# Kernel tuning notes

Measured on AMD Instinct MI355X. Metric: run time of the kernel, lower is better.

## Reference

```python
import jax, jax.numpy as jnp
import numpy as np

M = 1024   # memory_length
C = 1024   # context_length
H = 16     # num_heads
HD = 64    # head_dim = features // num_heads


def _relative_shift(x):
    # x: [B, H, T, K] -> Transformer-XL relative shift trick
    b, h, q_len, k_len = x.shape
    x = jnp.pad(x, ((0, 0), (0, 0), (0, 0), (1, 0)))
    x = x.reshape(b, h, k_len + 1, q_len)[:, :, 1:, :]
    return x.reshape(b, h, q_len, k_len)


def setup_inputs() -> dict:
    key = jax.random.key(0)
    ks = jax.random.split(key, 12)
    B, T, F = 2, C, H * HD
    S = M + C
    w = 0.02  # init scale for params
    return {
        "x": jax.random.normal(ks[0], (B, T, F), jnp.float32),
        "mask": jnp.zeros((B, T), jnp.int32),
        "mem_state": jax.random.normal(ks[1], (B, M, F), jnp.float32),
        "mem_mask": jnp.zeros((B, M), jnp.int32),
        "cache_key": jax.random.normal(ks[2], (B, C, H, HD), jnp.float32),
        "cache_value": jax.random.normal(ks[3], (B, C, H, HD), jnp.float32),
        "cache_mask": jnp.zeros((B, C), jnp.int32),
        "rel_emb": jax.random.normal(ks[4], (S, F), jnp.float32),
        "Wq": jax.random.normal(ks[5], (F, H, HD), jnp.float32) * w,
        "Wk": jax.random.normal(ks[6], (F, H, HD), jnp.float32) * w,
        "Wv": jax.random.normal(ks[7], (F, H, HD), jnp.float32) * w,
        "Wr": jax.random.normal(ks[8], (F, H, HD), jnp.float32) * w,
        "u": jax.random.normal(ks[9], (H, HD), jnp.float32) * w,
        "v": jax.random.normal(ks[10], (H, HD), jnp.float32) * w,
        "Wo": jax.random.normal(ks[11], (H, HD, F), jnp.float32) * w,
    }


def reference(x, mask, mem_state, mem_mask, cache_key, cache_value, cache_mask,
              rel_emb, Wq, Wk, Wv, Wr, u, v, Wo):
    B, T, F = x.shape
    S = M + C
    scale = 1.0 / jnp.sqrt(jnp.float32(HD))

    # projections
    q = jnp.einsum('btf,fnh->btnh', x, Wq)                       # [B,T,H,hd]
    kv_in = jnp.concatenate([mem_state, x], axis=1)              # [B,M+T,F]
    k = jnp.einsum('bsf,fnh->bsnh', kv_in, Wk)
    k = jnp.concatenate([k[:, :-T], cache_key, k[:, -T:]], axis=1)[:, -S:]   # [B,S,H,hd]
    val = jnp.einsum('bsf,fnh->bsnh', kv_in, Wv)
    val = jnp.concatenate([val[:, :-T], cache_value, val[:, -T:]], axis=1)[:, -S:]
    r = jnp.einsum('mf,fnh->mnh', rel_emb, Wr)                   # [S,H,hd]

    # relative position bias (shift trick), already scaled by 1/sqrt(hd)
    bd = jnp.einsum('btnh,mnh->bntm', q + v[None, None], r)      # [B,H,T,S]
    bd = _relative_shift(bd)[..., -S:]
    bias = bd * scale

    # segment mask from cumsum of start flags
    q_seg = jnp.cumsum(mask.astype(jnp.int32), axis=1) + \
        jnp.max(jnp.cumsum(jnp.concatenate([mem_mask, cache_mask], axis=1), axis=1), axis=1)[:, None]
    k_seg = jnp.cumsum(jnp.concatenate([mem_mask, cache_mask, mask], axis=1).astype(jnp.int32), axis=1)[:, -S:]
    seg_mask = q_seg[:, None, :, None] == k_seg[:, None, None, :]   # [B,1,T,S]

    # causal mask over absolute positions
    q_pos = jnp.arange(T) + S
    k_pos = jnp.arange(S + T)[-S:]
    causal = q_pos[:, None] >= k_pos[None, :]                    # [T,S]
    full_mask = seg_mask & causal[None, None]                    # [B,1,T,S] broadcast to H

    logits = jnp.einsum('btnh,bsnh->bnts', q + u[None, None], k) * scale + bias
    logits = jnp.where(full_mask, logits, jnp.float32(-1e30))
    attn = jax.nn.softmax(logits, axis=-1)                       # [B,H,T,S]

    o = jnp.einsum('bnts,bsnh->btnh', attn, val)
    out = jnp.einsum('btnh,nhf->btf', o, Wo)                     # [B,T,F]

    new_key = k[:, -C:]
    new_value = val[:, -C:]
    return out, new_key, new_value
```

## Files before the change

### kernel.cpp

```cpp
#include <hip/hip_runtime.h>
#include <hip/hip_bf16.h>
#include <climits>


typedef unsigned short u16;
typedef short bf16x8 __attribute__((ext_vector_type(8)));
typedef float f32x4 __attribute__((ext_vector_type(4)));

__device__ __forceinline__ f32x4 mfma16x16x32(bf16x8 a, bf16x8 b, f32x4 c) {
  return __builtin_amdgcn_mfma_f32_16x16x32_bf16(a, b, c, 0, 0, 0);
}

__device__ __forceinline__ u16 f2bf(float f) {
  __hip_bfloat16 h = __float2bfloat16(f);
  return *reinterpret_cast<u16*>(&h);
}

__device__ __forceinline__ float bf2f(u16 x) {
  unsigned u = ((unsigned)x) << 16;
  return __builtin_bit_cast(float, u);
}

__device__ __forceinline__ void gll16(const void* g, void* l) {
  __builtin_amdgcn_global_load_lds(
      (const __attribute__((address_space(1))) void*)g,
      (__attribute__((address_space(3))) void*)l, 16, 0, 0);
}

template <int CTRL>
__device__ __forceinline__ float rot16(float x) {
  int i = __builtin_bit_cast(int, x);
  int r = __builtin_amdgcn_update_dpp(i, i, CTRL, 0xF, 0xF, false);
  return __builtin_bit_cast(float, r);
}
__device__ __forceinline__ float dpp_max16(float x) {
  x = fmaxf(x, rot16<0x128>(x));
  x = fmaxf(x, rot16<0x124>(x));
  x = fmaxf(x, rot16<0x122>(x));
  x = fmaxf(x, rot16<0x121>(x));
  return x;
}
__device__ __forceinline__ float dpp_sum16(float x) {
  x += rot16<0x128>(x);
  x += rot16<0x124>(x);
  x += rot16<0x122>(x);
  x += rot16<0x121>(x);
  return x;
}

__global__ __launch_bounds__(64) void seg_scan_kernel(
    const int* __restrict__ mask, const int* __restrict__ mem_mask,
    const int* __restrict__ cache_mask, int* __restrict__ qseg,
    int* __restrict__ kseg) {
  __shared__ int cs[3072];
  int b = blockIdx.x, lane = threadIdx.x;
  int carry = 0;
  for (int base = 0; base < 3072; base += 64) {
    int idx = base + lane;
    int val;
    if (idx < 1024)      val = mem_mask[b * 1024 + idx];
    else if (idx < 2048) val = cache_mask[b * 1024 + idx - 1024];
    else                 val = mask[b * 1024 + idx - 2048];
    for (int o = 1; o < 64; o <<= 1) {
      int n = __shfl_up(val, o);
      if (lane >= o) val += n;
    }
    val += carry;
    cs[idx] = val;
    carry = __shfl(val, 63);
  }
  __syncthreads();
  int mx = INT_MIN;
  for (int i = lane; i < 2048; i += 64) mx = max(mx, cs[i]);
  for (int o = 1; o < 64; o <<= 1) mx = max(mx, __shfl_xor(mx, o));
  int cs2047 = cs[2047];
  for (int t = lane; t < 1024; t += 64) qseg[b * 1024 + t] = cs[2048 + t] - cs2047 + mx;
  for (int j = lane; j < 2048; j += 64) kseg[b * 2048 + j] = cs[1024 + j];
}

__global__ __launch_bounds__(256) void cvt2_kernel(const float* __restrict__ s0,
                                                   u16* __restrict__ d0,
                                                   const float* __restrict__ s1,
                                                   u16* __restrict__ d1) {
  int q = blockIdx.x * 256 + threadIdx.x;
  const float* s;
  u16* d;
  int i;
  if (q < 524288) { s = s0; d = d0; i = q * 4; }
  else            { s = s1; d = d1; i = (q - 524288) * 4; }
  float4 v = *(const float4*)(s + i);
  d[i + 0] = f2bf(v.x); d[i + 1] = f2bf(v.y);
  d[i + 2] = f2bf(v.z); d[i + 3] = f2bf(v.w);
}

__global__ __launch_bounds__(256) void tr_w5_kernel(
    const float* __restrict__ Wq, const float* __restrict__ Wk,
    const float* __restrict__ Wv, const float* __restrict__ Wr,
    const float* __restrict__ Wo, u16* __restrict__ wt5) {
  __shared__ float tile[32][33];
  int z = blockIdx.z;
  const float* src = (z == 0) ? Wq : (z == 1) ? Wk : (z == 2) ? Wv
                     : (z == 3) ? Wr : Wo;
  u16* dst = wt5 + ((size_t)z << 20);
  int tx = threadIdx.x & 31, ty = threadIdx.x >> 5;
  int r0 = blockIdx.y * 32, c0 = blockIdx.x * 32;
#pragma unroll
  for (int i = 0; i < 32; i += 8)
    tile[ty + i][tx] = src[(size_t)(r0 + ty + i) * 1024 + c0 + tx];
  __syncthreads();
#pragma unroll
  for (int i = 0; i < 32; i += 8)
    dst[(size_t)(c0 + ty + i) * 1024 + r0 + tx] = f2bf(tile[tx][ty + i]);
}

__global__ __launch_bounds__(256) void ck_perm_kernel(const float* __restrict__ src,
                                                      u16* __restrict__ dst) {
  int i = blockIdx.x * 256 + threadIdx.x;
  int dq = i & 15, h = (i >> 4) & 15, t = (i >> 8) & 1023, b = i >> 18;
  float4 v = *(const float4*)(src + (size_t)i * 4);
  size_t o = (((size_t)(b * 16 + h)) * 2048 + t) * 64 + dq * 4;
  dst[o + 0] = f2bf(v.x); dst[o + 1] = f2bf(v.y);
  dst[o + 2] = f2bf(v.z); dst[o + 3] = f2bf(v.w);
}

__global__ __launch_bounds__(256) void cv_tr_kernel(const float* __restrict__ src,
                                                    u16* __restrict__ dst) {
  __shared__ float tile[32][33];
  int bh = blockIdx.z, b = bh >> 4, h = bh & 15;
  int t0 = blockIdx.x * 32, d0 = blockIdx.y * 32;
  int tx = threadIdx.x & 31, ty = threadIdx.x >> 5;
#pragma unroll
  for (int i = 0; i < 32; i += 8)
    tile[ty + i][tx] = src[(((size_t)b * 1024 + t0 + ty + i) * 16 + h) * 64 + d0 + tx];
  __syncthreads();
#pragma unroll
  for (int i = 0; i < 32; i += 8)
    dst[((size_t)bh * 64 + d0 + ty + i) * 2048 + t0 + tx] = f2bf(tile[tx][ty + i]);
}

__global__ __launch_bounds__(256, 2) void gemm_proj_kernel(
    const u16* __restrict__ xbf, const u16* __restrict__ relbf,
    const u16* __restrict__ obf, const u16* __restrict__ wt5,
    u16* __restrict__ qu, u16* __restrict__ qv, u16* __restrict__ kbuf,
    u16* __restrict__ vtbuf, u16* __restrict__ rbuf, float* __restrict__ dout,
    const float* __restrict__ uvec, const float* __restrict__ vvec, int movr) {
  __shared__ __align__(16) u16 lA[128 * 64];
  __shared__ __align__(16) u16 lB[128 * 64];
  const int mode = (movr >= 0) ? movr : (int)blockIdx.z;
  const u16* A = (mode == 3) ? relbf : ((mode == 4) ? obf : xbf);
  const u16* Wm = wt5 + (size_t)mode * 1048576;
  const int tid = threadIdx.x;
  const int lane = tid & 63, gq = lane >> 4, cl = lane & 15;
  const int wv = tid >> 6, wm = wv >> 1, wn = wv & 1;
  const int by = blockIdx.y * 128, bx = blockIdx.x * 128;
  const f32x4 fz = {0.f, 0.f, 0.f, 0.f};

  f32x4 acc[4][4];
#pragma unroll
  for (int mi = 0; mi < 4; ++mi)
#pragma unroll
    for (int ni = 0; ni < 4; ++ni) acc[mi][ni] = fz;

  int offs[4];
  const u16 *pA[4], *pB[4];
#pragma unroll
  for (int c = 0; c < 4; ++c) {
    int off = tid * 16 + c * 4096;
    int L = off ^ (((off >> 7) & 7) << 4);
    int rr = off >> 7, ke = (L & 127) >> 1;
    offs[c] = off;
    pA[c] = A + (size_t)(by + rr) * 1024 + ke;
    pB[c] = Wm + (size_t)(bx + rr) * 1024 + ke;
  }

  for (int k0 = 0; k0 < 1024; k0 += 64) {
#pragma unroll
    for (int c = 0; c < 4; ++c) {
      gll16(pA[c] + k0, (char*)lA + offs[c]);
      gll16(pB[c] + k0, (char*)lB + offs[c]);
    }
    __syncthreads();
    bf16x8 af[4][2], bff[4][2];
#pragma unroll
    for (int mi = 0; mi < 4; ++mi)
#pragma unroll
      for (int kb = 0; kb < 2; ++kb) {
        int row = wm * 64 + mi * 16 + cl;
        int byte = row * 128 + kb * 64 + gq * 16;
        byte ^= ((row & 7) << 4);
        af[mi][kb] = *(const bf16x8*)((const char*)lA + byte);
      }
#pragma unroll
    for (int ni = 0; ni < 4; ++ni)
#pragma unroll
      for (int kb = 0; kb < 2; ++kb) {
        int row = wn * 64 + ni * 16 + cl;
        int byte = row * 128 + kb * 64 + gq * 16;
        byte ^= ((row & 7) << 4);
        bff[ni][kb] = *(const bf16x8*)((const char*)lB + byte);
      }
#pragma unroll
    for (int mi = 0; mi < 4; ++mi)
#pragma unroll
      for (int ni = 0; ni < 4; ++ni) {
        acc[mi][ni] = mfma16x16x32(af[mi][0], bff[ni][0], acc[mi][ni]);
        acc[mi][ni] = mfma16x16x32(af[mi][1], bff[ni][1], acc[mi][ni]);
      }
    __syncthreads();
  }

  const float SC = 0.18033688011112042f;
#pragma unroll
  for (int mi = 0; mi < 4; ++mi)
#pragma unroll
    for (int ni = 0; ni < 4; ++ni) {
      int n = bx + wn * 64 + ni * 16 + cl;
      float ub = 0.f, vb = 0.f;
      if (mode == 0) { ub = uvec[n]; vb = vvec[n]; }
#pragma unroll
      for (int r = 0; r < 4; ++r) {
        int m = by + wm * 64 + mi * 16 + 4 * gq + r;
        float val = acc[mi][ni][r];
        if (mode == 0) {
          qu[(size_t)m * 1024 + n] = f2bf((val + ub) * SC);
          qv[(size_t)m * 1024 + n] = f2bf((val + vb) * SC);
        } else if (mode == 1) {
          dout[2097152 + (size_t)m * 1024 + n] = val;
          kbuf[(((size_t)((m >> 10) * 16 + (n >> 6))) * 2048 + 1024 + (m & 1023)) * 64 +
               (n & 63)] = f2bf(val);
        } else if (mode == 2) {
          dout[4194304 + (size_t)m * 1024 + n] = val;
          vtbuf[(((size_t)((m >> 10) * 16 + (n >> 6))) * 64 + (n & 63)) * 2048 + 1024 +
                (m & 1023)] = f2bf(val);
        } else if (mode == 3) {
          rbuf[((size_t)(n >> 6) * 2048 + m) * 64 + (n & 63)] = f2bf(val);
        } else {
          dout[(size_t)m * 1024 + n] = val;
        }
      }
    }
}

__global__ __launch_bounds__(256, 2) void attn_kernel(
    const u16* __restrict__ qu, const u16* __restrict__ qv,
    const u16* __restrict__ kbuf, const u16* __restrict__ vtbuf,
    const u16* __restrict__ rbuf, const int* __restrict__ qseg,
    const int* __restrict__ kseg, u16* __restrict__ pO,
    float* __restrict__ pml) {
  __shared__ __align__(16) u16 ldsK[2][64 * 64];
  __shared__ __align__(16) u16 ldsV[2][64 * 64];
  __shared__ __align__(16) u16 ldsP[4][16 * 64];

  const int tid = threadIdx.x, lane = tid & 63;
  const int gq = lane >> 4, cl = lane & 15;
  const int wv = tid >> 6;
  int lin = blockIdx.x + 64 * blockIdx.y;
  lin = (lin & 7) * 256 + (lin >> 3);
  const int bh = lin >> 6, xx = lin & 63;
  const int qt = xx >> 2, chunk = xx & 3;
  const int b = bh >> 4, h = bh & 15;
  const int i0b = qt * 64;
  const int i0 = i0b + wv * 16;
  const int tmax = (i0b + 63 + 1024) >> 6;
  const f32x4 fz = {0.f, 0.f, 0.f, 0.f};

  const u16* rbh = rbuf + (size_t)h * 2048 * 64;
  const int* ksegb = kseg + (size_t)b * 2048;

  const u16* Kbase = kbuf + (size_t)bh * 2048 * 64;
  const u16* Vbase = vtbuf + (size_t)bh * 64 * 2048;
  const int offc0 = tid * 16, offc1 = tid * 16 + 4096;
  const int L0s = offc0 ^ (((offc0 >> 7) & 7) << 4);
  const int L1s = offc1 ^ (((offc1 >> 7) & 7) << 4);
  const u16* kS0 = Kbase + (size_t)(offc0 >> 7) * 64 + ((L0s & 127) >> 1);
  const u16* kS1 = Kbase + (size_t)(offc1 >> 7) * 64 + ((L1s & 127) >> 1);
  const u16* vS0 = Vbase + (size_t)(offc0 >> 7) * 2048 + ((L0s & 127) >> 1);
  const u16* vS1 = Vbase + (size_t)(offc1 >> 7) * 2048 + ((L1s & 127) >> 1);

#define STAGE(T, B)                                                \
  do {                                                             \
    gll16(kS0 + (size_t)(T) * 4096, (char*)ldsK[B] + offc0);       \
    gll16(kS1 + (size_t)(T) * 4096, (char*)ldsK[B] + offc1);       \
    gll16(vS0 + (T) * 64, (char*)ldsV[B] + offc0);                 \
    gll16(vS1 + (T) * 64, (char*)ldsV[B] + offc1);                 \
  } while (0)

  STAGE(chunk, 0);

  bf16x8 aU[2], aV[2];
#pragma unroll
  for (int kb = 0; kb < 2; ++kb) {
    size_t off = ((size_t)b * 1024 + i0 + cl) * 1024 + h * 64 + kb * 32 + gq * 8;
    aU[kb] = *(const bf16x8*)(qu + off);
    aV[kb] = *(const bf16x8*)(qv + off);
  }
  int qsv[4], srcl[4], athr[4];
  bool sel[4];
#pragma unroll
  for (int r = 0; r < 4; ++r) {
    int ri = 4 * gq + r;
    qsv[r] = qseg[b * 1024 + i0 + ri];
    int lc = cl - ri + 15;
    srcl[r] = (gq << 4) | (lc & 15);
    sel[r] = (lc < 16);
    athr[r] = i0 + ri + 1024 - cl;
  }

  float mrun[4], lrun[4];
  f32x4 oacc[4];
#pragma unroll
  for (int r = 0; r < 4; ++r) { mrun[r] = -1e30f; lrun[r] = 0.f; }
#pragma unroll
  for (int di = 0; di < 4; ++di) oacc[di] = fz;

  __syncthreads();

  int bufi = 0;
  for (int t = chunk; t <= tmax; t += 4, bufi ^= 1) {
    if (t + 4 <= tmax) STAGE(t + 4, bufi ^ 1);
    const int j0t = t * 64;
    const int Rb0 = j0t - i0 + 1008;
    bf16x8 Rf[5][2];
#pragma unroll
    for (int p = 0; p < 5; ++p) {
      const u16* rp = rbh + (size_t)min(Rb0 + 16 * p + cl, 2047) * 64 + gq * 8;
      Rf[p][0] = *(const bf16x8*)rp;
      Rf[p][1] = *(const bf16x8*)(rp + 32);
    }
    int ksv[4];
#pragma unroll
    for (int jt = 0; jt < 4; ++jt) ksv[jt] = ksegb[j0t + 16 * jt + cl];
    __builtin_amdgcn_sched_barrier(0);

    const char* Kl = (const char*)ldsK[bufi];
    const char* Vl = (const char*)ldsV[bufi];
    f32x4 xq[4];
#pragma unroll
    for (int jt = 0; jt < 4; ++jt) {
      int row = jt * 16 + cl;
      int sw = (row & 7) << 4;
      bf16x8 k0 = *(const bf16x8*)(Kl + ((row * 128 + gq * 16) ^ sw));
      bf16x8 k1 = *(const bf16x8*)(Kl + ((row * 128 + 64 + gq * 16) ^ sw));
      f32x4 a = mfma16x16x32(aU[0], k0, fz);
      xq[jt] = mfma16x16x32(aU[1], k1, a);
    }
    f32x4 bb[5];
#pragma unroll
    for (int p = 0; p < 5; ++p) {
      f32x4 a = mfma16x16x32(aV[0], Rf[p][0], fz);
      bb[p] = mfma16x16x32(aV[1], Rf[p][1], a);
    }
    float D[5][4];
#pragma unroll
    for (int p = 0; p < 5; ++p)
#pragma unroll
      for (int r = 0; r < 4; ++r) D[p][r] = __shfl(bb[p][r], srcl[r]);
    __builtin_amdgcn_sched_barrier(0);

    float x[4][4];
#pragma unroll
    for (int jt = 0; jt < 4; ++jt)
#pragma unroll
      for (int r = 0; r < 4; ++r) {
        float bdv = sel[r] ? D[jt][r] : D[jt + 1][r];
        bool ok = (j0t + 16 * jt <= athr[r]) && (ksv[jt] == qsv[r]);
        x[jt][r] = ok ? (xq[jt][r] + bdv) : -1e30f;
      }

    char* Pm = (char*)ldsP[wv];
    float alf[4];
#pragma unroll
    for (int r = 0; r < 4; ++r) {
      float mx = fmaxf(fmaxf(x[0][r], x[1][r]), fmaxf(x[2][r], x[3][r]));
      mx = dpp_max16(mx);
      float mold = mrun[r];
      float mnew = fmaxf(mold, mx);
      float al = exp2f(mold - mnew);
      float p0 = exp2f(x[0][r] - mnew);
      float p1 = exp2f(x[1][r] - mnew);
      float p2 = exp2f(x[2][r] - mnew);
      float p3 = exp2f(x[3][r] - mnew);
      float s = dpp_sum16(p0 + p1 + p2 + p3);
      mrun[r] = mnew;
      lrun[r] = lrun[r] * al + s;
      alf[r] = al;
      int ri = 4 * gq + r;
      int bbx = (ri & 7) << 4;
      *(u16*)(Pm + ((ri * 128 + cl * 2) ^ bbx)) = f2bf(p0);
      *(u16*)(Pm + ((ri * 128 + (16 + cl) * 2) ^ bbx)) = f2bf(p1);
      *(u16*)(Pm + ((ri * 128 + (32 + cl) * 2) ^ bbx)) = f2bf(p2);
      *(u16*)(Pm + ((ri * 128 + (48 + cl) * 2) ^ bbx)) = f2bf(p3);
    }
    f32x4 av = {alf[0], alf[1], alf[2], alf[3]};
#pragma unroll
    for (int di = 0; di < 4; ++di) oacc[di] *= av;
    int psw = (cl & 7) << 4;
    bf16x8 pf0 = *(const bf16x8*)(Pm + ((cl * 128 + gq * 16) ^ psw));
    bf16x8 pf1 = *(const bf16x8*)(Pm + ((cl * 128 + 64 + gq * 16) ^ psw));
#pragma unroll
    for (int di = 0; di < 4; ++di) {
      int row = di * 16 + cl;
      int sw = (row & 7) << 4;
      bf16x8 v0 = *(const bf16x8*)(Vl + ((row * 128 + gq * 16) ^ sw));
      bf16x8 v1 = *(const bf16x8*)(Vl + ((row * 128 + 64 + gq * 16) ^ sw));
      oacc[di] = mfma16x16x32(pf0, v0, oacc[di]);
      oacc[di] = mfma16x16x32(pf1, v1, oacc[di]);
    }
    __syncthreads();
  }
#undef STAGE

#pragma unroll
  for (int r = 0; r < 4; ++r) {
    int iq = i0 + 4 * gq + r;
    size_t rowp = ((size_t)bh * 4 + chunk) * 1024 + iq;
#pragma unroll
    for (int di = 0; di < 4; ++di)
      __builtin_nontemporal_store(f2bf(oacc[di][r]), &pO[rowp * 64 + di * 16 + cl]);
    if (cl == 0) {
      __builtin_nontemporal_store(mrun[r], &pml[rowp * 2]);
      __builtin_nontemporal_store(lrun[r], &pml[rowp * 2 + 1]);
    }
  }
}

__global__ __launch_bounds__(256) void combine_kernel(
    const u16* __restrict__ pO, const float* __restrict__ pml,
    u16* __restrict__ obf) {
  int gid = blockIdx.x * 256 + threadIdx.x;
  int d8 = (gid & 7) * 8;
  int row = gid >> 3;
  int bh = row >> 10, iq = row & 1023;
  int b = bh >> 4, h = bh & 15;
  size_t rbase = (size_t)bh * 4 * 1024 + iq;
  float m[4], l[4], w[4];
  float ms = -1e30f;
#pragma unroll
  for (int c = 0; c < 4; ++c) {
    m[c] = pml[(rbase + c * 1024) * 2];
    l[c] = pml[(rbase + c * 1024) * 2 + 1];
    ms = fmaxf(ms, m[c]);
  }
  float den = 0.f;
#pragma unroll
  for (int c = 0; c < 4; ++c) { w[c] = exp2f(m[c] - ms); den += l[c] * w[c]; }
  float inv = 1.0f / fmaxf(den, 1e-30f);
  float acc[8] = {0, 0, 0, 0, 0, 0, 0, 0};
#pragma unroll
  for (int c = 0; c < 4; ++c) {
    bf16x8 a = *(const bf16x8*)(pO + (rbase + c * 1024) * 64 + d8);
#pragma unroll
    for (int j = 0; j < 8; ++j) acc[j] += bf2f((u16)a[j]) * w[c];
  }
  bf16x8 o;
#pragma unroll
  for (int j = 0; j < 8; ++j) o[j] = (short)f2bf(acc[j] * inv);
  *(bf16x8*)(obf + ((size_t)b * 1024 + iq) * 1024 + h * 64 + d8) = o;
}

extern "C" void kernel_launch(void* const* d_in, const int* in_sizes, int n_in,
                              void* d_out, int out_size, void* d_ws, size_t ws_size,
                              hipStream_t stream) {
  (void)in_sizes; (void)n_in; (void)out_size; (void)ws_size;
  const float* x           = (const float*)d_in[0];
  const int*   mask        = (const int*)d_in[1];
  const int*   mem_mask    = (const int*)d_in[3];
  const float* cache_key   = (const float*)d_in[4];
  const float* cache_value = (const float*)d_in[5];
  const int*   cache_mask  = (const int*)d_in[6];
  const float* rel_emb     = (const float*)d_in[7];
  const float* Wq          = (const float*)d_in[8];
  const float* Wk          = (const float*)d_in[9];
  const float* Wv          = (const float*)d_in[10];
  const float* Wr          = (const float*)d_in[11];
  const float* uvec        = (const float*)d_in[12];
  const float* vvec        = (const float*)d_in[13];
  const float* Wo          = (const float*)d_in[14];
  float* dout = (float*)d_out;

  char* W = (char*)d_ws;
  u16* xbf   = (u16*)(W + (0u << 20));
  u16* relbf = (u16*)(W + (4u << 20));
  u16* pO    = (u16*)(W + (0u << 20));
  u16* wt5   = (u16*)(W + (8u << 20));
  u16* kbuf  = (u16*)(W + (18u << 20));
  u16* vtbuf = (u16*)(W + (26u << 20));
  u16* rbuf  = (u16*)(W + (34u << 20));
  u16* qu    = (u16*)(W + (38u << 20));
  u16* qv    = (u16*)(W + (42u << 20));
  u16* obf   = (u16*)(W + (46u << 20));
  int* qseg  = (int*)(W + (50u << 20));
  int* kseg  = (int*)(W + (50u << 20) + 8192);
  float* pml = (float*)(W + (50u << 20) + 32768);

  seg_scan_kernel<<<dim3(2), dim3(64), 0, stream>>>(mask, mem_mask, cache_mask, qseg, kseg);
  cvt2_kernel<<<dim3(4096), dim3(256), 0, stream>>>(x, xbf, rel_emb, relbf);
  tr_w5_kernel<<<dim3(32, 32, 5), dim3(256), 0, stream>>>(Wq, Wk, Wv, Wr, Wo, wt5);
  ck_perm_kernel<<<dim3(2048), dim3(256), 0, stream>>>(cache_key, kbuf);
  cv_tr_kernel<<<dim3(32, 2, 32), dim3(256), 0, stream>>>(cache_value, vtbuf);
  gemm_proj_kernel<<<dim3(8, 16, 4), dim3(256), 0, stream>>>(
      xbf, relbf, obf, wt5, qu, qv, kbuf, vtbuf, rbuf, dout, uvec, vvec, -1);
  attn_kernel<<<dim3(64, 32), dim3(256), 0, stream>>>(qu, qv, kbuf, vtbuf, rbuf,
                                                      qseg, kseg, pO, pml);
  combine_kernel<<<dim3(1024), dim3(256), 0, stream>>>(pO, pml, obf);
  gemm_proj_kernel<<<dim3(8, 16, 1), dim3(256), 0, stream>>>(
      xbf, relbf, obf, wt5, qu, qv, kbuf, vtbuf, rbuf, dout, uvec, vvec, 4);
}
```

Measured before the change: 197.1 us.

## Widen attention blocks to 128 queries, add dedicated 64x64 output-projection GEMM

The attention kernel now uses 512 threads (8 waves) per block, so each block covers 128 query rows and every staged K/V tile is shared by twice as many waves. It also skips the causal comparison on tiles that lie fully inside the causal region, and raises wave priority around the MFMA sections. The output projection moves to its own 64x64-tile GEMM kernel with a 512-block grid, so the small M=2048 GEMM occupies more CUs than the 128-tile generic kernel did. In exchange, the larger attention block needs more LDS and registers per block, which may lower occupancy, and the new GEMM has no double buffering.

```diff
diff --git a/kernel.cpp b/kernel.cpp
--- a/kernel.cpp
+++ b/kernel.cpp
@@ -140,14 +140,14 @@
 
 __global__ __launch_bounds__(256, 2) void gemm_proj_kernel(
     const u16* __restrict__ xbf, const u16* __restrict__ relbf,
-    const u16* __restrict__ obf, const u16* __restrict__ wt5,
-    u16* __restrict__ qu, u16* __restrict__ qv, u16* __restrict__ kbuf,
-    u16* __restrict__ vtbuf, u16* __restrict__ rbuf, float* __restrict__ dout,
-    const float* __restrict__ uvec, const float* __restrict__ vvec, int movr) {
+    const u16* __restrict__ wt5, u16* __restrict__ qu, u16* __restrict__ qv,
+    u16* __restrict__ kbuf, u16* __restrict__ vtbuf, u16* __restrict__ rbuf,
+    float* __restrict__ dout, const float* __restrict__ uvec,
+    const float* __restrict__ vvec) {
   __shared__ __align__(16) u16 lA[128 * 64];
   __shared__ __align__(16) u16 lB[128 * 64];
-  const int mode = (movr >= 0) ? movr : (int)blockIdx.z;
-  const u16* A = (mode == 3) ? relbf : ((mode == 4) ? obf : xbf);
+  const int mode = (int)blockIdx.z;
+  const u16* A = (mode == 3) ? relbf : xbf;
   const u16* Wm = wt5 + (size_t)mode * 1048576;
   const int tid = threadIdx.x;
   const int lane = tid & 63, gq = lane >> 4, cl = lane & 15;
@@ -232,16 +232,89 @@
           dout[4194304 + (size_t)m * 1024 + n] = val;
           vtbuf[(((size_t)((m >> 10) * 16 + (n >> 6))) * 64 + (n & 63)) * 2048 + 1024 +
                 (m & 1023)] = f2bf(val);
-        } else if (mode == 3) {
+        } else {
           rbuf[((size_t)(n >> 6) * 2048 + m) * 64 + (n & 63)] = f2bf(val);
-        } else {
-          dout[(size_t)m * 1024 + n] = val;
         }
       }
     }
 }
 
-__global__ __launch_bounds__(256, 2) void attn_kernel(
+__global__ __launch_bounds__(256, 2) void gemm_o_kernel(
+    const u16* __restrict__ obf, const u16* __restrict__ wo,
+    float* __restrict__ dout) {
+  __shared__ __align__(16) u16 lA[64 * 64];
+  __shared__ __align__(16) u16 lB[64 * 64];
+  const int tid = threadIdx.x;
+  const int lane = tid & 63, gq = lane >> 4, cl = lane & 15;
+  const int wv = tid >> 6, wm = wv >> 1, wn = wv & 1;
+  const int by = blockIdx.y * 64, bx = blockIdx.x * 64;
+  const f32x4 fz = {0.f, 0.f, 0.f, 0.f};
+
+  f32x4 acc[2][2];
+#pragma unroll
+  for (int a = 0; a < 2; ++a)
+#pragma unroll
+    for (int bq = 0; bq < 2; ++bq) acc[a][bq] = fz;
+
+  const int off0 = tid * 16, off1 = tid * 16 + 4096;
+  const int L0 = off0 ^ (((off0 >> 7) & 7) << 4);
+  const int L1 = off1 ^ (((off1 >> 7) & 7) << 4);
+  const int rr0 = off0 >> 7, ke0 = (L0 & 127) >> 1;
+  const int rr1 = off1 >> 7, ke1 = (L1 & 127) >> 1;
+  const u16* pA0 = obf + (size_t)(by + rr0) * 1024 + ke0;
+  const u16* pA1 = obf + (size_t)(by + rr1) * 1024 + ke1;
+  const u16* pB0 = wo + (size_t)(bx + rr0) * 1024 + ke0;
+  const u16* pB1 = wo + (size_t)(bx + rr1) * 1024 + ke1;
+
+  for (int k0 = 0; k0 < 1024; k0 += 64) {
+    gll16(pA0 + k0, (char*)lA + off0);
+    gll16(pA1 + k0, (char*)lA + off1);
+    gll16(pB0 + k0, (char*)lB + off0);
+    gll16(pB1 + k0, (char*)lB + off1);
+    __syncthreads();
+    bf16x8 af[2][2], bff[2][2];
+#pragma unroll
+    for (int mi = 0; mi < 2; ++mi)
+#pragma unroll
+      for (int kb = 0; kb < 2; ++kb) {
+        int row = wm * 32 + mi * 16 + cl;
+        int byte = row * 128 + kb * 64 + gq * 16;
+        byte ^= ((row & 7) << 4);
+        af[mi][kb] = *(const bf16x8*)((const char*)lA + byte);
+      }
+#pragma unroll
+    for (int ni = 0; ni < 2; ++ni)
+#pragma unroll
+      for (int kb = 0; kb < 2; ++kb) {
+        int row = wn * 32 + ni * 16 + cl;
+        int byte = row * 128 + kb * 64 + gq * 16;
+        byte ^= ((row & 7) << 4);
+        bff[ni][kb] = *(const bf16x8*)((const char*)lB + byte);
+      }
+#pragma unroll
+    for (int mi = 0; mi < 2; ++mi)
+#pragma unroll
+      for (int ni = 0; ni < 2; ++ni) {
+        acc[mi][ni] = mfma16x16x32(af[mi][0], bff[ni][0], acc[mi][ni]);
+        acc[mi][ni] = mfma16x16x32(af[mi][1], bff[ni][1], acc[mi][ni]);
+      }
+    __syncthreads();
+  }
+
+#pragma unroll
+  for (int mi = 0; mi < 2; ++mi)
+#pragma unroll
+    for (int ni = 0; ni < 2; ++ni) {
+      int n = bx + wn * 32 + ni * 16 + cl;
+#pragma unroll
+      for (int r = 0; r < 4; ++r) {
+        int m = by + wm * 32 + mi * 16 + 4 * gq + r;
+        dout[(size_t)m * 1024 + n] = acc[mi][ni][r];
+      }
+    }
+}
+
+__global__ __launch_bounds__(512, 2) void attn_kernel(
     const u16* __restrict__ qu, const u16* __restrict__ qv,
     const u16* __restrict__ kbuf, const u16* __restrict__ vtbuf,
     const u16* __restrict__ rbuf, const int* __restrict__ qseg,
@@ -249,19 +322,19 @@
     float* __restrict__ pml) {
   __shared__ __align__(16) u16 ldsK[2][64 * 64];
   __shared__ __align__(16) u16 ldsV[2][64 * 64];
-  __shared__ __align__(16) u16 ldsP[4][16 * 64];
+  __shared__ __align__(16) u16 ldsP[8][16 * 64];
 
   const int tid = threadIdx.x, lane = tid & 63;
   const int gq = lane >> 4, cl = lane & 15;
   const int wv = tid >> 6;
-  int lin = blockIdx.x + 64 * blockIdx.y;
-  lin = (lin & 7) * 256 + (lin >> 3);
-  const int bh = lin >> 6, xx = lin & 63;
-  const int qt = xx >> 2, chunk = xx & 3;
+  int lin = blockIdx.x + 32 * blockIdx.y;
+  lin = (lin & 7) * 128 + (lin >> 3);
+  const int bh = lin >> 5, xx = lin & 31;
+  const int qb = xx >> 2, chunk = xx & 3;
   const int b = bh >> 4, h = bh & 15;
-  const int i0b = qt * 64;
+  const int i0b = qb * 128;
   const int i0 = i0b + wv * 16;
-  const int tmax = (i0b + 63 + 1024) >> 6;
+  const int tmax = (i0b + 127 + 1024) >> 6;
   const f32x4 fz = {0.f, 0.f, 0.f, 0.f};
 
   const u16* rbh = rbuf + (size_t)h * 2048 * 64;
@@ -269,20 +342,15 @@
 
   const u16* Kbase = kbuf + (size_t)bh * 2048 * 64;
   const u16* Vbase = vtbuf + (size_t)bh * 64 * 2048;
-  const int offc0 = tid * 16, offc1 = tid * 16 + 4096;
-  const int L0s = offc0 ^ (((offc0 >> 7) & 7) << 4);
-  const int L1s = offc1 ^ (((offc1 >> 7) & 7) << 4);
-  const u16* kS0 = Kbase + (size_t)(offc0 >> 7) * 64 + ((L0s & 127) >> 1);
-  const u16* kS1 = Kbase + (size_t)(offc1 >> 7) * 64 + ((L1s & 127) >> 1);
-  const u16* vS0 = Vbase + (size_t)(offc0 >> 7) * 2048 + ((L0s & 127) >> 1);
-  const u16* vS1 = Vbase + (size_t)(offc1 >> 7) * 2048 + ((L1s & 127) >> 1);
-
-#define STAGE(T, B)                                                \
-  do {                                                             \
-    gll16(kS0 + (size_t)(T) * 4096, (char*)ldsK[B] + offc0);       \
-    gll16(kS1 + (size_t)(T) * 4096, (char*)ldsK[B] + offc1);       \
-    gll16(vS0 + (T) * 64, (char*)ldsV[B] + offc0);                 \
-    gll16(vS1 + (T) * 64, (char*)ldsV[B] + offc1);                 \
+  const int offc = tid * 16;
+  const int Ls = offc ^ (((offc >> 7) & 7) << 4);
+  const u16* kS = Kbase + (size_t)(offc >> 7) * 64 + ((Ls & 127) >> 1);
+  const u16* vS = Vbase + (size_t)(offc >> 7) * 2048 + ((Ls & 127) >> 1);
+
+#define STAGE(T, B)                                          \
+  do {                                                       \
+    gll16(kS + (size_t)(T) * 4096, (char*)ldsK[B] + offc);   \
+    gll16(vS + (T) * 64, (char*)ldsV[B] + offc);             \
   } while (0)
 
   STAGE(chunk, 0);
@@ -320,6 +388,7 @@
     if (t + 4 <= tmax) STAGE(t + 4, bufi ^ 1);
     const int j0t = t * 64;
     const int Rb0 = j0t - i0 + 1008;
+    const bool interior = (j0t + 63 <= i0 + 1024);
     bf16x8 Rf[5][2];
 #pragma unroll
     for (int p = 0; p < 5; ++p) {
@@ -334,6 +403,7 @@
 
     const char* Kl = (const char*)ldsK[bufi];
     const char* Vl = (const char*)ldsV[bufi];
+    __builtin_amdgcn_s_setprio(1);
     f32x4 xq[4];
 #pragma unroll
     for (int jt = 0; jt < 4; ++jt) {
@@ -350,6 +420,7 @@
       f32x4 a = mfma16x16x32(aV[0], Rf[p][0], fz);
       bb[p] = mfma16x16x32(aV[1], Rf[p][1], a);
     }
+    __builtin_amdgcn_s_setprio(0);
     float D[5][4];
 #pragma unroll
     for (int p = 0; p < 5; ++p)
@@ -363,7 +434,7 @@
 #pragma unroll
       for (int r = 0; r < 4; ++r) {
         float bdv = sel[r] ? D[jt][r] : D[jt + 1][r];
-        bool ok = (j0t + 16 * jt <= athr[r]) && (ksv[jt] == qsv[r]);
+        bool ok = (interior || (j0t + 16 * jt <= athr[r])) && (ksv[jt] == qsv[r]);
         x[jt][r] = ok ? (xq[jt][r] + bdv) : -1e30f;
       }
 
@@ -397,6 +468,7 @@
     int psw = (cl & 7) << 4;
     bf16x8 pf0 = *(const bf16x8*)(Pm + ((cl * 128 + gq * 16) ^ psw));
     bf16x8 pf1 = *(const bf16x8*)(Pm + ((cl * 128 + 64 + gq * 16) ^ psw));
+    __builtin_amdgcn_s_setprio(1);
 #pragma unroll
     for (int di = 0; di < 4; ++di) {
       int row = di * 16 + cl;
@@ -406,6 +478,7 @@
       oacc[di] = mfma16x16x32(pf0, v0, oacc[di]);
       oacc[di] = mfma16x16x32(pf1, v1, oacc[di]);
     }
+    __builtin_amdgcn_s_setprio(0);
     __syncthreads();
   }
 #undef STAGE
@@ -499,10 +572,9 @@
   ck_perm_kernel<<<dim3(2048), dim3(256), 0, stream>>>(cache_key, kbuf);
   cv_tr_kernel<<<dim3(32, 2, 32), dim3(256), 0, stream>>>(cache_value, vtbuf);
   gemm_proj_kernel<<<dim3(8, 16, 4), dim3(256), 0, stream>>>(
-      xbf, relbf, obf, wt5, qu, qv, kbuf, vtbuf, rbuf, dout, uvec, vvec, -1);
-  attn_kernel<<<dim3(64, 32), dim3(256), 0, stream>>>(qu, qv, kbuf, vtbuf, rbuf,
+      xbf, relbf, wt5, qu, qv, kbuf, vtbuf, rbuf, dout, uvec, vvec);
+  attn_kernel<<<dim3(32, 32), dim3(512), 0, stream>>>(qu, qv, kbuf, vtbuf, rbuf,
                                                       qseg, kseg, pO, pml);
   combine_kernel<<<dim3(1024), dim3(256), 0, stream>>>(pO, pml, obf);
-  gemm_proj_kernel<<<dim3(8, 16, 1), dim3(256), 0, stream>>>(
-      xbf, relbf, obf, wt5, qu, qv, kbuf, vtbuf, rbuf, dout, uvec, vvec, 4);
-}
+  gemm_o_kernel<<<dim3(16, 32), dim3(256), 0, stream>>>(obf, wt5 + (4u << 20), dout);
+}
```

Result: slower. 224.9 us (+14.1%).
